# Kernel optimization log

Hardware: AMD Instinct MI355X
Metric: run time of the kernel (lower is better)

## Reference

```python
import jax, jax.numpy as jnp
import numpy as np

N = 50000   # nodes
E = 800000  # edges
F_IN, F_HID, F_OUT = 128, 96, 40


def setup_inputs() -> dict:
    key = jax.random.key(0)
    ks = jax.random.split(key, 9)
    x = jax.random.normal(ks[0], (N, F_IN), dtype=jnp.float32)
    edge_index = jax.random.randint(ks[1], (2, E), 0, N, dtype=jnp.int32)
    def lin(k, fi, fo):
        s = 1.0 / np.sqrt(fi)
        return jax.random.uniform(k, (fi, fo), jnp.float32, -s, s)
    W1 = lin(ks[2], F_IN, F_HID)
    b1 = jnp.zeros((F_HID,), jnp.float32)
    W2 = lin(ks[3], F_HID, F_HID)
    b2 = jnp.zeros((F_HID,), jnp.float32)
    Wout = lin(ks[4], F_HID, F_OUT)
    bout = jnp.zeros((F_OUT,), jnp.float32)
    return {"x": x, "edge_index": edge_index, "W1": W1, "b1": b1,
            "W2": W2, "b2": b2, "Wout": Wout, "bout": bout}


def _gcn_norm(edge_index, n):
    # add self-loops, symmetric degree normalization (PyG GCNConv default)
    loops = jnp.arange(n, dtype=edge_index.dtype)
    src = jnp.concatenate([edge_index[0], loops])
    dst = jnp.concatenate([edge_index[1], loops])
    deg = jax.ops.segment_sum(jnp.ones_like(dst, dtype=jnp.float32), dst,
                              num_segments=n)
    dinv = jnp.where(deg > 0, jax.lax.rsqrt(deg), 0.0)
    norm = dinv[src] * dinv[dst]   # [E+N]
    return src, dst, norm


def _gcn_layer(h, src, dst, norm, W, b, n):
    # linear transform, then normalized scatter-add aggregation, then bias
    h = h @ W                                 # [N, Fout]
    msg = h[src] * norm[:, None]              # gather + scale
    agg = jax.ops.segment_sum(msg, dst, num_segments=n)
    return agg + b


def reference(x, edge_index, W1, b1, W2, b2, Wout, bout):
    n = x.shape[0]
    src, dst, norm = _gcn_norm(edge_index, n)
    h = jax.nn.relu(_gcn_layer(x, src, dst, norm, W1, b1, n))
    h = jax.nn.relu(_gcn_layer(h, src, dst, norm, W2, b2, n))
    return h @ Wout + bout
```

## Files before the change

kernel.cpp:

```cpp
#include <hip/hip_runtime.h>
#include <hip/hip_fp16.h>

#define N_NODES 50000
#define N_EDGES 800000
#define F_INN   128
#define F_HID   96
#define F_OUTT  40

typedef _Float16 half8 __attribute__((ext_vector_type(8)));
typedef float    floatx4 __attribute__((ext_vector_type(4)));


__global__ void count_kernel(const int* __restrict__ dst, int* __restrict__ counts4,
                             int* __restrict__ rank, int e) {
    int i = blockIdx.x * blockDim.x + threadIdx.x;
    if (i < e) rank[i] = atomicAdd(&counts4[dst[i] * 4 + (i & 3)], 1);
}

__global__ __launch_bounds__(1024) void scan_local_kernel(
        const int4* __restrict__ counts4, int* __restrict__ row_start,
        float* __restrict__ dinv, int* __restrict__ blk_sums, int n) {
    __shared__ int wave_sums[16];
    int tid = threadIdx.x, lane = tid & 63, wid = tid >> 6;
    int i = blockIdx.x * 1024 + tid;
    int v = 0;
    if (i < n) {
        int4 c = counts4[i];
        v = c.x + c.y + c.z + c.w;
    }
    int val = v;
    #pragma unroll
    for (int off = 1; off < 64; off <<= 1) {
        int u = __shfl_up(val, off, 64);
        if (lane >= off) val += u;
    }
    if (lane == 63) wave_sums[wid] = val;
    __syncthreads();
    if (wid == 0) {
        int w = (lane < 16) ? wave_sums[lane] : 0;
        #pragma unroll
        for (int off = 1; off < 16; off <<= 1) {
            int u = __shfl_up(w, off, 64);
            if (lane >= off) w += u;
        }
        if (lane < 16) wave_sums[lane] = w;
    }
    __syncthreads();
    int excl = ((wid == 0) ? 0 : wave_sums[wid - 1]) + (val - v);
    if (i < n) {
        row_start[i] = excl;
        dinv[i] = rsqrtf((float)(v + 1));
    }
    if (tid == 0) blk_sums[blockIdx.x] = wave_sums[15];
}

__global__ void scan_blk_kernel(const int* __restrict__ blk_sums, int* __restrict__ blk_off,
                                int* __restrict__ row_start, int n, int nblk) {
    int lane = threadIdx.x;
    int v = (lane < nblk) ? blk_sums[lane] : 0;
    int val = v;
    #pragma unroll
    for (int off = 1; off < 64; off <<= 1) {
        int u = __shfl_up(val, off, 64);
        if (lane >= off) val += u;
    }
    if (lane < nblk) blk_off[lane] = val - v;
    if (lane == 63) row_start[n] = val;
}

__global__ __launch_bounds__(1024) void scan_apply_kernel(
        int* __restrict__ row_start, const int* __restrict__ blk_off,
        const int4* __restrict__ counts4, int4* __restrict__ base4, int n) {
    int i = blockIdx.x * 1024 + threadIdx.x;
    if (i >= n) return;
    int4 c = counts4[i];
    int b = row_start[i] + blk_off[blockIdx.x];
    row_start[i] = b;
    base4[i] = make_int4(b, b + c.x, b + c.x + c.y, b + c.x + c.y + c.z);
}

__global__ void fill_csr_kernel(const int* __restrict__ src, const int* __restrict__ dst,
                                const int* __restrict__ rank, const int* __restrict__ base4,
                                int* __restrict__ csr_src, int e) {
    int i = blockIdx.x * blockDim.x + threadIdx.x;
    if (i >= e) return;
    csr_src[base4[dst[i] * 4 + (i & 3)] + rank[i]] = src[i];
}

__global__ void wt_kernel(const float* __restrict__ W1, const float* __restrict__ W2,
                          __half* __restrict__ BT1, __half* __restrict__ BT2) {
    int i = blockIdx.x * 256 + threadIdx.x;
    if (i < 96 * 128) {
        int j = i / 128, k = i - j * 128;
        BT1[j * 136 + k] = __float2half(W1[k * 96 + j]);
    } else if (i < 96 * 128 + 96 * 96) {
        int t = i - 96 * 128;
        int j = t / 96, k = t - j * 96;
        BT2[j * 136 + k] = __float2half(W2[k * 96 + j]);
    }
}

template <int FI>
__global__ __launch_bounds__(256) void mfma_gemm_kernel(
        const float* __restrict__ X, const __half* __restrict__ BTg,
        const float* __restrict__ dinv, float4* __restrict__ Th4, int n) {
    __shared__ __half BTl[96 * 136];
    __shared__ __half OUTl[4 * 16 * 104];
    int tid = threadIdx.x;
    {
        const int4* s = reinterpret_cast<const int4*>(BTg);
        int4* d = reinterpret_cast<int4*>(BTl);
        for (int i = tid; i < 96 * 136 / 8; i += 256) d[i] = s[i];
    }
    __syncthreads();

    int lane = tid & 63, w = tid >> 6;
    int lm = lane & 15, q = lane >> 4;
    int base = blockIdx.x * 64 + w * 16;
    int node = base + lm;
    int nclamp = min(node, n - 1);
    const float* Xrow = X + (size_t)nclamp * FI;

    floatx4 cf[6];
    #pragma unroll
    for (int t = 0; t < 6; ++t) cf[t] = (floatx4){0.f, 0.f, 0.f, 0.f};

    constexpr int KS = FI / 32;
    #pragma unroll
    for (int ks = 0; ks < KS; ++ks) {
        const float4* xr = reinterpret_cast<const float4*>(Xrow + 32 * ks + q * 8);
        float4 f0 = xr[0], f1 = xr[1];
        union { half8 v; __half2 h[4]; } b;
        b.h[0] = __floats2half2_rn(f0.x, f0.y);
        b.h[1] = __floats2half2_rn(f0.z, f0.w);
        b.h[2] = __floats2half2_rn(f1.x, f1.y);
        b.h[3] = __floats2half2_rn(f1.z, f1.w);
        #pragma unroll
        for (int t = 0; t < 6; ++t) {
            half8 a = *reinterpret_cast<const half8*>(
                &BTl[(t * 16 + lm) * 136 + q * 8 + 32 * ks]);
            cf[t] = __builtin_amdgcn_mfma_f32_16x16x32_f16(a, b.v, cf[t], 0, 0, 0);
        }
    }

    float dn = dinv[nclamp];
    __half* orow = OUTl + (w * 16 + lm) * 104;
    #pragma unroll
    for (int t = 0; t < 6; ++t) {
        union { int2 i2; __half2 h[2]; } u;
        u.h[0] = __floats2half2_rn(cf[t][0] * dn, cf[t][1] * dn);
        u.h[1] = __floats2half2_rn(cf[t][2] * dn, cf[t][3] * dn);
        *reinterpret_cast<int2*>(&orow[t * 16 + q * 4]) = u.i2;
    }
    #pragma unroll
    for (int R = 0; R < 3; ++R) {
        int nl = lane >> 2, c = (lane & 3) + 4 * R;
        float4 v = *reinterpret_cast<const float4*>(&OUTl[(w * 16 + nl) * 104 + c * 8]);
        int gn = base + nl;
        if (gn < n) Th4[(size_t)gn * 12 + c] = v;
    }
}

__global__ __launch_bounds__(320) void gemm_out_kernel(
        const float* __restrict__ A, const float* __restrict__ W,
        const float* __restrict__ bias, float* __restrict__ C, int n) {
    __shared__ float Wlds[96 * 40];
    int tid = threadIdx.y * 10 + threadIdx.x;
    for (int i = tid; i < 96 * 10; i += 320)
        reinterpret_cast<float4*>(Wlds)[i] = reinterpret_cast<const float4*>(W)[i];
    __syncthreads();

    int j    = threadIdx.x * 4;
    int node = blockIdx.x * 32 + threadIdx.y;
    int nc   = min(node, n - 1);
    float4 acc = make_float4(0.f, 0.f, 0.f, 0.f);
    for (int k = 0; k < 96; k += 4) {
        float4 a = *reinterpret_cast<const float4*>(A + (size_t)nc * 96 + k);
        float4 w0 = *reinterpret_cast<const float4*>(Wlds + (k + 0) * 40 + j);
        float4 w1 = *reinterpret_cast<const float4*>(Wlds + (k + 1) * 40 + j);
        float4 w2 = *reinterpret_cast<const float4*>(Wlds + (k + 2) * 40 + j);
        float4 w3 = *reinterpret_cast<const float4*>(Wlds + (k + 3) * 40 + j);
        acc.x += a.x * w0.x + a.y * w1.x + a.z * w2.x + a.w * w3.x;
        acc.y += a.x * w0.y + a.y * w1.y + a.z * w2.y + a.w * w3.y;
        acc.z += a.x * w0.z + a.y * w1.z + a.z * w2.z + a.w * w3.z;
        acc.w += a.x * w0.w + a.y * w1.w + a.z * w2.w + a.w * w3.w;
    }
    if (node < n) {
        float4 b = *reinterpret_cast<const float4*>(bias + j);
        acc.x += b.x; acc.y += b.y; acc.z += b.z; acc.w += b.w;
        *reinterpret_cast<float4*>(C + (size_t)node * 40 + j) = acc;
    }
}

__global__ __launch_bounds__(256) void agg_kernel(
        const __half2* __restrict__ T, const int* __restrict__ row_start,
        const int* __restrict__ csr_src, const float* __restrict__ dinv,
        const float* __restrict__ bias, float* __restrict__ H, int n) {
    int lane = threadIdx.x & 63;
    int node = __builtin_amdgcn_readfirstlane(blockIdx.x * 4 + (threadIdx.x >> 6));
    if (node >= n) return;
    int fl = min(lane, 47);

    float2 self = __half22float2(T[(size_t)node * 48 + fl]);
    float accx = self.x, accy = self.y;

    int idx = row_start[node];
    int end = row_start[node + 1];
    for (; idx + 8 <= end; idx += 8) {
        int s[8];
        #pragma unroll
        for (int u = 0; u < 8; ++u) s[u] = csr_src[idx + u];
        float2 f[8];
        #pragma unroll
        for (int u = 0; u < 8; ++u) f[u] = __half22float2(T[(size_t)s[u] * 48 + fl]);
        #pragma unroll
        for (int u = 0; u < 8; ++u) { accx += f[u].x; accy += f[u].y; }
    }
    for (; idx < end; ++idx) {
        float2 f = __half22float2(T[(size_t)csr_src[idx] * 48 + fl]);
        accx += f.x; accy += f.y;
    }
    if (lane < 48) {
        float dn = dinv[node];
        float2 b = reinterpret_cast<const float2*>(bias)[lane];
        float2 o;
        o.x = fmaxf(dn * accx + b.x, 0.f);
        o.y = fmaxf(dn * accy + b.y, 0.f);
        reinterpret_cast<float2*>(H)[(size_t)node * 48 + lane] = o;
    }
}


extern "C" void kernel_launch(void* const* d_in, const int* in_sizes, int n_in,
                              void* d_out, int out_size, void* d_ws, size_t ws_size,
                              hipStream_t stream) {
    const float* x    = (const float*)d_in[0];
    const int*   ei   = (const int*)d_in[1];
    const float* W1   = (const float*)d_in[2];
    const float* b1   = (const float*)d_in[3];
    const float* W2   = (const float*)d_in[4];
    const float* b2   = (const float*)d_in[5];
    const float* Wout = (const float*)d_in[6];
    const float* bout = (const float*)d_in[7];
    float*       out  = (float*)d_out;

    const int* src = ei;
    const int* dst = ei + N_EDGES;

    char* ws = (char*)d_ws;
    size_t off = 0;
    auto alloc = [&](size_t bytes) {
        size_t o = off;
        off = (off + bytes + 511) & ~(size_t)511;
        return (void*)(ws + o);
    };
    int*     counts4   = (int*)    alloc((size_t)N_NODES * 4 * sizeof(int));
    int4*    base4     = (int4*)   alloc((size_t)N_NODES * sizeof(int4));
    int*     row_start = (int*)    alloc((N_NODES + 1) * sizeof(int));
    float*   dinv      = (float*)  alloc(N_NODES * sizeof(float));
    int*     blk_sums  = (int*)    alloc(64 * sizeof(int));
    int*     blk_off   = (int*)    alloc(64 * sizeof(int));
    int*     rank      = (int*)    alloc((size_t)N_EDGES * sizeof(int));
    int*     csr_src   = (int*)    alloc((size_t)N_EDGES * sizeof(int));
    __half*  BT1       = (__half*) alloc((size_t)96 * 136 * sizeof(__half));
    __half*  BT2       = (__half*) alloc((size_t)96 * 136 * sizeof(__half));
    __half2* Th        = (__half2*)alloc((size_t)N_NODES * 48 * sizeof(__half2));
    float*   Hf        = (float*)  alloc((size_t)N_NODES * F_HID * sizeof(float));

    const int NSCAN = (N_NODES + 1023) / 1024;

    wt_kernel<<<(96 * 128 + 96 * 96 + 255) / 256, 256, 0, stream>>>(W1, W2, BT1, BT2);

    hipMemsetAsync(counts4, 0, (size_t)N_NODES * 4 * sizeof(int), stream);
    count_kernel<<<(N_EDGES + 255) / 256, 256, 0, stream>>>(dst, counts4, rank, N_EDGES);
    scan_local_kernel<<<NSCAN, 1024, 0, stream>>>(
        (const int4*)counts4, row_start, dinv, blk_sums, N_NODES);
    scan_blk_kernel<<<1, 64, 0, stream>>>(blk_sums, blk_off, row_start, N_NODES, NSCAN);
    scan_apply_kernel<<<NSCAN, 1024, 0, stream>>>(
        row_start, blk_off, (const int4*)counts4, base4, N_NODES);
    fill_csr_kernel<<<(N_EDGES + 255) / 256, 256, 0, stream>>>(
        src, dst, rank, (const int*)base4, csr_src, N_EDGES);

    mfma_gemm_kernel<F_INN><<<(N_NODES + 63) / 64, 256, 0, stream>>>(
        x, BT1, dinv, (float4*)Th, N_NODES);
    agg_kernel<<<(N_NODES + 3) / 4, 256, 0, stream>>>(
        Th, row_start, csr_src, dinv, b1, Hf, N_NODES);

    mfma_gemm_kernel<F_HID><<<(N_NODES + 63) / 64, 256, 0, stream>>>(
        Hf, BT2, dinv, (float4*)Th, N_NODES);
    agg_kernel<<<(N_NODES + 3) / 4, 256, 0, stream>>>(
        Th, row_start, csr_src, dinv, b2, Hf, N_NODES);

    gemm_out_kernel<<<(N_NODES + 31) / 32, dim3(10, 32), 0, stream>>>(
        Hf, Wout, bout, out, N_NODES);
}
```

Measured before the change: 232.6 us.

## Fuse edge counting with first GEMM, fold block scan, store hidden activations in fp16

```diff
diff --git a/kernel.cpp b/kernel.cpp
--- a/kernel.cpp
+++ b/kernel.cpp
@@ -10,11 +10,102 @@
 typedef _Float16 half8 __attribute__((ext_vector_type(8)));
 typedef float    floatx4 __attribute__((ext_vector_type(4)));
 
-
-__global__ void count_kernel(const int* __restrict__ dst, int* __restrict__ counts4,
-                             int* __restrict__ rank, int e) {
-    int i = blockIdx.x * blockDim.x + threadIdx.x;
-    if (i < e) rank[i] = atomicAdd(&counts4[dst[i] * 4 + (i & 3)], 1);
+template <int FI, typename TIN>
+__device__ __forceinline__ void mfma_gemm_body(
+        const TIN* __restrict__ X, const __half* __restrict__ BTg,
+        float4* __restrict__ Th4, int n, int bx) {
+    __shared__ __half BTl[96 * 136];
+    __shared__ __half OUTl[4 * 16 * 104];
+    int tid = threadIdx.x;
+    {
+        const int4* s = reinterpret_cast<const int4*>(BTg);
+        int4* d = reinterpret_cast<int4*>(BTl);
+        for (int i = tid; i < 96 * 136 / 8; i += 256) d[i] = s[i];
+    }
+    __syncthreads();
+
+    int lane = tid & 63, w = tid >> 6;
+    int lm = lane & 15, q = lane >> 4;
+    int base = bx * 64 + w * 16;
+    int node = base + lm;
+    int nclamp = min(node, n - 1);
+    const TIN* Xrow = X + (size_t)nclamp * FI;
+
+    floatx4 cf[6];
+    #pragma unroll
+    for (int t = 0; t < 6; ++t) cf[t] = (floatx4){0.f, 0.f, 0.f, 0.f};
+
+    constexpr int KS = FI / 32;
+    #pragma unroll
+    for (int ks = 0; ks < KS; ++ks) {
+        half8 bv;
+        if constexpr (sizeof(TIN) == 4) {
+            const float4* xr = reinterpret_cast<const float4*>(Xrow + 32 * ks + q * 8);
+            float4 f0 = xr[0], f1 = xr[1];
+            union { half8 v; __half2 h[4]; } b;
+            b.h[0] = __floats2half2_rn(f0.x, f0.y);
+            b.h[1] = __floats2half2_rn(f0.z, f0.w);
+            b.h[2] = __floats2half2_rn(f1.x, f1.y);
+            b.h[3] = __floats2half2_rn(f1.z, f1.w);
+            bv = b.v;
+        } else {
+            bv = *reinterpret_cast<const half8*>(Xrow + 32 * ks + q * 8);
+        }
+        #pragma unroll
+        for (int t = 0; t < 6; ++t) {
+            half8 a = *reinterpret_cast<const half8*>(
+                &BTl[(t * 16 + lm) * 136 + q * 8 + 32 * ks]);
+            cf[t] = __builtin_amdgcn_mfma_f32_16x16x32_f16(a, bv, cf[t], 0, 0, 0);
+        }
+    }
+
+    __half* orow = OUTl + (w * 16 + lm) * 104;
+    #pragma unroll
+    for (int t = 0; t < 6; ++t) {
+        union { int2 i2; __half2 h[2]; } u;
+        u.h[0] = __floats2half2_rn(cf[t][0], cf[t][1]);
+        u.h[1] = __floats2half2_rn(cf[t][2], cf[t][3]);
+        *reinterpret_cast<int2*>(&orow[t * 16 + q * 4]) = u.i2;
+    }
+    #pragma unroll
+    for (int R = 0; R < 3; ++R) {
+        int nl = lane >> 2, c = (lane & 3) + 4 * R;
+        float4 v = *reinterpret_cast<const float4*>(&OUTl[(w * 16 + nl) * 104 + c * 8]);
+        int gn = base + nl;
+        if (gn < n) Th4[(size_t)gn * 12 + c] = v;
+    }
+}
+
+__global__ __launch_bounds__(256) void count_gemm1_kernel(
+        const int* __restrict__ dst, int* __restrict__ counts4, int* __restrict__ rank,
+        int e, const float* __restrict__ X, const __half* __restrict__ BT1,
+        float4* __restrict__ Th4, int n, int nCB) {
+    if ((int)blockIdx.x < nCB) {
+        int i = blockIdx.x * 256 + threadIdx.x;
+        if (i < e) rank[i] = atomicAdd(&counts4[dst[i] * 4 + (i & 3)], 1);
+    } else {
+        mfma_gemm_body<F_INN, float>(X, BT1, Th4, n, blockIdx.x - nCB);
+    }
+}
+
+template <int FI, typename TIN>
+__global__ __launch_bounds__(256) void mfma_gemm_kernel(
+        const TIN* __restrict__ X, const __half* __restrict__ BTg,
+        float4* __restrict__ Th4, int n) {
+    mfma_gemm_body<FI, TIN>(X, BTg, Th4, n, blockIdx.x);
+}
+
+__global__ void wt_kernel(const float* __restrict__ W1, const float* __restrict__ W2,
+                          __half* __restrict__ BT1, __half* __restrict__ BT2) {
+    int i = blockIdx.x * 256 + threadIdx.x;
+    if (i < 96 * 128) {
+        int j = i / 128, k = i - j * 128;
+        BT1[j * 136 + k] = __float2half(W1[k * 96 + j]);
+    } else if (i < 96 * 128 + 96 * 96) {
+        int t = i - 96 * 128;
+        int j = t / 96, k = t - j * 96;
+        BT2[j * 136 + k] = __float2half(W2[k * 96 + j]);
+    }
 }
 
 __global__ __launch_bounds__(1024) void scan_local_kernel(
@@ -54,29 +145,31 @@
     if (tid == 0) blk_sums[blockIdx.x] = wave_sums[15];
 }
 
-__global__ void scan_blk_kernel(const int* __restrict__ blk_sums, int* __restrict__ blk_off,
-                                int* __restrict__ row_start, int n, int nblk) {
-    int lane = threadIdx.x;
-    int v = (lane < nblk) ? blk_sums[lane] : 0;
-    int val = v;
-    #pragma unroll
-    for (int off = 1; off < 64; off <<= 1) {
-        int u = __shfl_up(val, off, 64);
-        if (lane >= off) val += u;
-    }
-    if (lane < nblk) blk_off[lane] = val - v;
-    if (lane == 63) row_start[n] = val;
-}
-
 __global__ __launch_bounds__(1024) void scan_apply_kernel(
-        int* __restrict__ row_start, const int* __restrict__ blk_off,
-        const int4* __restrict__ counts4, int4* __restrict__ base4, int n) {
-    int i = blockIdx.x * 1024 + threadIdx.x;
-    if (i >= n) return;
-    int4 c = counts4[i];
-    int b = row_start[i] + blk_off[blockIdx.x];
-    row_start[i] = b;
-    base4[i] = make_int4(b, b + c.x, b + c.x + c.y, b + c.x + c.y + c.z);
+        int* __restrict__ row_start, const int* __restrict__ blk_sums,
+        const int4* __restrict__ counts4, int4* __restrict__ base4, int n, int nblk) {
+    __shared__ int s_my, s_tot;
+    int tid = threadIdx.x;
+    if (tid < 64) {
+        int v = (tid < nblk) ? blk_sums[tid] : 0;
+        int val = v;
+        #pragma unroll
+        for (int off = 1; off < 64; off <<= 1) {
+            int u = __shfl_up(val, off, 64);
+            if (tid >= off) val += u;
+        }
+        if (tid == (int)blockIdx.x) s_my = val - v;
+        if (tid == 63) s_tot = val;
+    }
+    __syncthreads();
+    int i = blockIdx.x * 1024 + tid;
+    if (i < n) {
+        int4 c = counts4[i];
+        int b = row_start[i] + s_my;
+        row_start[i] = b;
+        base4[i] = make_int4(b, b + c.x, b + c.x + c.y, b + c.x + c.y + c.z);
+    }
+    if (blockIdx.x == 0 && tid == 0) row_start[n] = s_tot;
 }
 
 __global__ void fill_csr_kernel(const int* __restrict__ src, const int* __restrict__ dst,
@@ -87,82 +180,54 @@
     csr_src[base4[dst[i] * 4 + (i & 3)] + rank[i]] = src[i];
 }
 
-__global__ void wt_kernel(const float* __restrict__ W1, const float* __restrict__ W2,
-                          __half* __restrict__ BT1, __half* __restrict__ BT2) {
-    int i = blockIdx.x * 256 + threadIdx.x;
-    if (i < 96 * 128) {
-        int j = i / 128, k = i - j * 128;
-        BT1[j * 136 + k] = __float2half(W1[k * 96 + j]);
-    } else if (i < 96 * 128 + 96 * 96) {
-        int t = i - 96 * 128;
-        int j = t / 96, k = t - j * 96;
-        BT2[j * 136 + k] = __float2half(W2[k * 96 + j]);
-    }
-}
-
-template <int FI>
-__global__ __launch_bounds__(256) void mfma_gemm_kernel(
-        const float* __restrict__ X, const __half* __restrict__ BTg,
-        const float* __restrict__ dinv, float4* __restrict__ Th4, int n) {
-    __shared__ __half BTl[96 * 136];
-    __shared__ __half OUTl[4 * 16 * 104];
-    int tid = threadIdx.x;
-    {
-        const int4* s = reinterpret_cast<const int4*>(BTg);
-        int4* d = reinterpret_cast<int4*>(BTl);
-        for (int i = tid; i < 96 * 136 / 8; i += 256) d[i] = s[i];
-    }
-    __syncthreads();
-
-    int lane = tid & 63, w = tid >> 6;
-    int lm = lane & 15, q = lane >> 4;
-    int base = blockIdx.x * 64 + w * 16;
-    int node = base + lm;
-    int nclamp = min(node, n - 1);
-    const float* Xrow = X + (size_t)nclamp * FI;
-
-    floatx4 cf[6];
-    #pragma unroll
-    for (int t = 0; t < 6; ++t) cf[t] = (floatx4){0.f, 0.f, 0.f, 0.f};
-
-    constexpr int KS = FI / 32;
-    #pragma unroll
-    for (int ks = 0; ks < KS; ++ks) {
-        const float4* xr = reinterpret_cast<const float4*>(Xrow + 32 * ks + q * 8);
-        float4 f0 = xr[0], f1 = xr[1];
-        union { half8 v; __half2 h[4]; } b;
-        b.h[0] = __floats2half2_rn(f0.x, f0.y);
-        b.h[1] = __floats2half2_rn(f0.z, f0.w);
-        b.h[2] = __floats2half2_rn(f1.x, f1.y);
-        b.h[3] = __floats2half2_rn(f1.z, f1.w);
-        #pragma unroll
-        for (int t = 0; t < 6; ++t) {
-            half8 a = *reinterpret_cast<const half8*>(
-                &BTl[(t * 16 + lm) * 136 + q * 8 + 32 * ks]);
-            cf[t] = __builtin_amdgcn_mfma_f32_16x16x32_f16(a, b.v, cf[t], 0, 0, 0);
-        }
-    }
-
-    float dn = dinv[nclamp];
-    __half* orow = OUTl + (w * 16 + lm) * 104;
-    #pragma unroll
-    for (int t = 0; t < 6; ++t) {
-        union { int2 i2; __half2 h[2]; } u;
-        u.h[0] = __floats2half2_rn(cf[t][0] * dn, cf[t][1] * dn);
-        u.h[1] = __floats2half2_rn(cf[t][2] * dn, cf[t][3] * dn);
-        *reinterpret_cast<int2*>(&orow[t * 16 + q * 4]) = u.i2;
-    }
-    #pragma unroll
-    for (int R = 0; R < 3; ++R) {
-        int nl = lane >> 2, c = (lane & 3) + 4 * R;
-        float4 v = *reinterpret_cast<const float4*>(&OUTl[(w * 16 + nl) * 104 + c * 8]);
-        int gn = base + nl;
-        if (gn < n) Th4[(size_t)gn * 12 + c] = v;
+__global__ __launch_bounds__(256) void agg_kernel(
+        const __half2* __restrict__ T, const int* __restrict__ row_start,
+        const int* __restrict__ csr_src, const float* __restrict__ dinv,
+        const float* __restrict__ bias, __half2* __restrict__ H, int n) {
+    int lane = threadIdx.x & 63;
+    int node = __builtin_amdgcn_readfirstlane(blockIdx.x * 4 + (threadIdx.x >> 6));
+    if (node >= n) return;
+    int fl = min(lane, 47);
+
+    float dn = dinv[node];
+    float2 self = __half22float2(T[(size_t)node * 48 + fl]);
+    float accx = dn * self.x, accy = dn * self.y;
+
+    int idx = row_start[node];
+    int end = row_start[node + 1];
+    for (; idx + 8 <= end; idx += 8) {
+        int s[8];
+        #pragma unroll
+        for (int u = 0; u < 8; ++u) s[u] = csr_src[idx + u];
+        float ws[8];
+        #pragma unroll
+        for (int u = 0; u < 8; ++u) ws[u] = dinv[s[u]];
+        float2 f[8];
+        #pragma unroll
+        for (int u = 0; u < 8; ++u) f[u] = __half22float2(T[(size_t)s[u] * 48 + fl]);
+        #pragma unroll
+        for (int u = 0; u < 8; ++u) {
+            accx = fmaf(ws[u], f[u].x, accx);
+            accy = fmaf(ws[u], f[u].y, accy);
+        }
+    }
+    for (; idx < end; ++idx) {
+        int s = csr_src[idx];
+        float w = dinv[s];
+        float2 f = __half22float2(T[(size_t)s * 48 + fl]);
+        accx = fmaf(w, f.x, accx);
+        accy = fmaf(w, f.y, accy);
+    }
+    if (lane < 48) {
+        float2 b = reinterpret_cast<const float2*>(bias)[lane];
+        float ox = fmaxf(fmaf(dn, accx, b.x), 0.f);
+        float oy = fmaxf(fmaf(dn, accy, b.y), 0.f);
+        H[(size_t)node * 48 + lane] = __floats2half2_rn(ox, oy);
     }
 }
 
 __global__ __launch_bounds__(320) void gemm_out_kernel(
-        const float* __restrict__ A, const float* __restrict__ W,
+        const __half2* __restrict__ A, const float* __restrict__ W,
         const float* __restrict__ bias, float* __restrict__ C, int n) {
     __shared__ float Wlds[96 * 40];
     int tid = threadIdx.y * 10 + threadIdx.x;
@@ -173,60 +238,25 @@
     int j    = threadIdx.x * 4;
     int node = blockIdx.x * 32 + threadIdx.y;
     int nc   = min(node, n - 1);
+    const __half2* Ah = A + (size_t)nc * 48;
     float4 acc = make_float4(0.f, 0.f, 0.f, 0.f);
-    for (int k = 0; k < 96; k += 4) {
-        float4 a = *reinterpret_cast<const float4*>(A + (size_t)nc * 96 + k);
+    for (int k2 = 0; k2 < 48; k2 += 2) {
+        float2 a01 = __half22float2(Ah[k2]);
+        float2 a23 = __half22float2(Ah[k2 + 1]);
+        int k = 2 * k2;
         float4 w0 = *reinterpret_cast<const float4*>(Wlds + (k + 0) * 40 + j);
         float4 w1 = *reinterpret_cast<const float4*>(Wlds + (k + 1) * 40 + j);
         float4 w2 = *reinterpret_cast<const float4*>(Wlds + (k + 2) * 40 + j);
         float4 w3 = *reinterpret_cast<const float4*>(Wlds + (k + 3) * 40 + j);
-        acc.x += a.x * w0.x + a.y * w1.x + a.z * w2.x + a.w * w3.x;
-        acc.y += a.x * w0.y + a.y * w1.y + a.z * w2.y + a.w * w3.y;
-        acc.z += a.x * w0.z + a.y * w1.z + a.z * w2.z + a.w * w3.z;
-        acc.w += a.x * w0.w + a.y * w1.w + a.z * w2.w + a.w * w3.w;
+        acc.x += a01.x * w0.x + a01.y * w1.x + a23.x * w2.x + a23.y * w3.x;
+        acc.y += a01.x * w0.y + a01.y * w1.y + a23.x * w2.y + a23.y * w3.y;
+        acc.z += a01.x * w0.z + a01.y * w1.z + a23.x * w2.z + a23.y * w3.z;
+        acc.w += a01.x * w0.w + a01.y * w1.w + a23.x * w2.w + a23.y * w3.w;
     }
     if (node < n) {
         float4 b = *reinterpret_cast<const float4*>(bias + j);
         acc.x += b.x; acc.y += b.y; acc.z += b.z; acc.w += b.w;
         *reinterpret_cast<float4*>(C + (size_t)node * 40 + j) = acc;
-    }
-}
-
-__global__ __launch_bounds__(256) void agg_kernel(
-        const __half2* __restrict__ T, const int* __restrict__ row_start,
-        const int* __restrict__ csr_src, const float* __restrict__ dinv,
-        const float* __restrict__ bias, float* __restrict__ H, int n) {
-    int lane = threadIdx.x & 63;
-    int node = __builtin_amdgcn_readfirstlane(blockIdx.x * 4 + (threadIdx.x >> 6));
-    if (node >= n) return;
-    int fl = min(lane, 47);
-
-    float2 self = __half22float2(T[(size_t)node * 48 + fl]);
-    float accx = self.x, accy = self.y;
-
-    int idx = row_start[node];
-    int end = row_start[node + 1];
-    for (; idx + 8 <= end; idx += 8) {
-        int s[8];
-        #pragma unroll
-        for (int u = 0; u < 8; ++u) s[u] = csr_src[idx + u];
-        float2 f[8];
-        #pragma unroll
-        for (int u = 0; u < 8; ++u) f[u] = __half22float2(T[(size_t)s[u] * 48 + fl]);
-        #pragma unroll
-        for (int u = 0; u < 8; ++u) { accx += f[u].x; accy += f[u].y; }
-    }
-    for (; idx < end; ++idx) {
-        float2 f = __half22float2(T[(size_t)csr_src[idx] * 48 + fl]);
-        accx += f.x; accy += f.y;
-    }
-    if (lane < 48) {
-        float dn = dinv[node];
-        float2 b = reinterpret_cast<const float2*>(bias)[lane];
-        float2 o;
-        o.x = fmaxf(dn * accx + b.x, 0.f);
-        o.y = fmaxf(dn * accy + b.y, 0.f);
-        reinterpret_cast<float2*>(H)[(size_t)node * 48 + lane] = o;
     }
 }
 
@@ -259,38 +289,38 @@
     int*     row_start = (int*)    alloc((N_NODES + 1) * sizeof(int));
     float*   dinv      = (float*)  alloc(N_NODES * sizeof(float));
     int*     blk_sums  = (int*)    alloc(64 * sizeof(int));
-    int*     blk_off   = (int*)    alloc(64 * sizeof(int));
     int*     rank      = (int*)    alloc((size_t)N_EDGES * sizeof(int));
     int*     csr_src   = (int*)    alloc((size_t)N_EDGES * sizeof(int));
     __half*  BT1       = (__half*) alloc((size_t)96 * 136 * sizeof(__half));
     __half*  BT2       = (__half*) alloc((size_t)96 * 136 * sizeof(__half));
     __half2* Th        = (__half2*)alloc((size_t)N_NODES * 48 * sizeof(__half2));
-    float*   Hf        = (float*)  alloc((size_t)N_NODES * F_HID * sizeof(float));
+    __half2* Hh        = (__half2*)alloc((size_t)N_NODES * 48 * sizeof(__half2));
 
     const int NSCAN = (N_NODES + 1023) / 1024;
-
+    const int CB    = (N_EDGES + 255) / 256;
+    const int GB    = (N_NODES + 63) / 64;
+
+    hipMemsetAsync(counts4, 0, (size_t)N_NODES * 4 * sizeof(int), stream);
     wt_kernel<<<(96 * 128 + 96 * 96 + 255) / 256, 256, 0, stream>>>(W1, W2, BT1, BT2);
 
-    hipMemsetAsync(counts4, 0, (size_t)N_NODES * 4 * sizeof(int), stream);
-    count_kernel<<<(N_EDGES + 255) / 256, 256, 0, stream>>>(dst, counts4, rank, N_EDGES);
+    count_gemm1_kernel<<<CB + GB, 256, 0, stream>>>(
+        dst, counts4, rank, N_EDGES, x, BT1, (float4*)Th, N_NODES, CB);
+
     scan_local_kernel<<<NSCAN, 1024, 0, stream>>>(
         (const int4*)counts4, row_start, dinv, blk_sums, N_NODES);
-    scan_blk_kernel<<<1, 64, 0, stream>>>(blk_sums, blk_off, row_start, N_NODES, NSCAN);
     scan_apply_kernel<<<NSCAN, 1024, 0, stream>>>(
-        row_start, blk_off, (const int4*)counts4, base4, N_NODES);
-    fill_csr_kernel<<<(N_EDGES + 255) / 256, 256, 0, stream>>>(
+        row_start, blk_sums, (const int4*)counts4, base4, N_NODES, NSCAN);
+    fill_csr_kernel<<<CB, 256, 0, stream>>>(
         src, dst, rank, (const int*)base4, csr_src, N_EDGES);
 
-    mfma_gemm_kernel<F_INN><<<(N_NODES + 63) / 64, 256, 0, stream>>>(
-        x, BT1, dinv, (float4*)Th, N_NODES);
     agg_kernel<<<(N_NODES + 3) / 4, 256, 0, stream>>>(
-        Th, row_start, csr_src, dinv, b1, Hf, N_NODES);
-
-    mfma_gemm_kernel<F_HID><<<(N_NODES + 63) / 64, 256, 0, stream>>>(
-        Hf, BT2, dinv, (float4*)Th, N_NODES);
+        Th, row_start, csr_src, dinv, b1, Hh, N_NODES);
+
+    mfma_gemm_kernel<F_HID, __half><<<GB, 256, 0, stream>>>(
+        (const __half*)Hh, BT2, (float4*)Th, N_NODES);
     agg_kernel<<<(N_NODES + 3) / 4, 256, 0, stream>>>(
-        Th, row_start, csr_src, dinv, b2, Hf, N_NODES);
+        Th, row_start, csr_src, dinv, b2, Hh, N_NODES);
 
     gemm_out_kernel<<<(N_NODES + 31) / 32, dim3(10, 32), 0, stream>>>(
-        Hf, Wout, bout, out, N_NODES);
-}
+        Hh, Wout, bout, out, N_NODES);
+}
```

Result: faster. 225.8 us (-2.9%).
